# Optimization experiments

Measured on AMD Instinct MI355X. Metric: run time of the kernel, lower is better.

Reference implementation:

```python
import jax, jax.numpy as jnp
import numpy as np

DIM = 768
HEADS = 12
HEAD_DIM = DIM // HEADS
SCALE = HEAD_DIM ** -0.5


def setup_inputs() -> dict:
    key = jax.random.key(0)
    k1, k2, k3, k4, k5 = jax.random.split(key, 5)
    B, N, C = 8, 1024, DIM
    x = jax.random.normal(k1, (B, N, C), dtype=jnp.float32)
    scale_emb = jax.random.normal(k2, (1, 1, C), dtype=jnp.float32)
    # nn.Linear weights stored as (out, in); bias only on proj
    w_qkv = jax.random.normal(k3, (3 * C, C), dtype=jnp.float32) * (C ** -0.5)
    w_proj = jax.random.normal(k4, (C, C), dtype=jnp.float32) * (C ** -0.5)
    b_proj = jax.random.normal(k5, (C,), dtype=jnp.float32) * 0.01
    return {"x": x, "scale_emb": scale_emb, "w_qkv": w_qkv, "w_proj": w_proj, "b_proj": b_proj}


def reference(x, scale_emb, w_qkv, w_proj, b_proj):
    B, N, C = x.shape
    H, D = HEADS, HEAD_DIM
    # qkv: (B, N, 3C) -> (3, B, H, N, D)
    qkv = jnp.einsum('bnc,oc->bno', x, w_qkv)
    qkv = qkv.reshape(B, N, 3, H, D).transpose(2, 0, 3, 1, 4)
    q, k, v = qkv[0], qkv[1], qkv[2]
    # scale_emb broadcast to (B, H, N, D) and added to k
    se = jnp.broadcast_to(scale_emb, (B, N, C)).reshape(B, N, H, D).transpose(0, 2, 1, 3)
    k = k + se
    attn_logits = jnp.einsum('bhnd,bhmd->bhnm', q, k) * SCALE
    attn_probs = jax.nn.softmax(attn_logits, axis=-1)
    out = jnp.einsum('bhnm,bhmd->bhnd', attn_probs, v)
    out = out.transpose(0, 2, 1, 3).reshape(B, N, C)
    out = jnp.einsum('bnc,oc->bno', out, w_proj) + b_proj
    return out, attn_probs
```

## Files before the change

kernel.cpp:

```cpp
#include <hip/hip_runtime.h>
#include <hip/hip_bf16.h>


typedef unsigned short u16;
typedef __attribute__((ext_vector_type(8))) short bf16x8;
typedef __attribute__((ext_vector_type(4))) float f32x4;

#define DEVI static __device__ __forceinline__

DEVI u16 f2bf(float f) {
  union { float f; unsigned int u; } v; v.f = f;
  return (u16)((v.u + 0x7fffu + ((v.u >> 16) & 1u)) >> 16);
}

DEVI void gload16(const void* g, void* l) {
  __builtin_amdgcn_global_load_lds(
      (const __attribute__((address_space(1))) unsigned int*)g,
      (__attribute__((address_space(3))) unsigned int*)l, 16, 0, 0);
}

__global__ void cvt_f32_bf16(const float* __restrict__ src, u16* __restrict__ dst, int n4) {
  int i = blockIdx.x * 256 + threadIdx.x;
  if (i >= n4) return;
  float4 f = ((const float4*)src)[i];
  unsigned int lo = f2bf(f.x) | ((unsigned int)f2bf(f.y) << 16);
  unsigned int hi = f2bf(f.z) | ((unsigned int)f2bf(f.w) << 16);
  ((uint2*)dst)[i] = make_uint2(lo, hi);
}

template<int MODE>
__global__ __launch_bounds__(256)
void gemm128(const u16* __restrict__ A, const u16* __restrict__ Bw, int K,
             const float* __restrict__ se,
             u16* __restrict__ qo, u16* __restrict__ ko, u16* __restrict__ vto,
             const float* __restrict__ bias, float* __restrict__ out)
{
  __shared__ u16 lA[128 * 32];
  __shared__ u16 lB[128 * 32];
  const int mt = blockIdx.x, nt = blockIdx.y;
  const int t = threadIdx.x;
  const int w = t >> 6, l = t & 63, lhi = l >> 4, llo = l & 15;
  const int wr = w >> 1, wc = w & 1;

  f32x4 acc[4][4];
#pragma unroll
  for (int m = 0; m < 4; ++m)
#pragma unroll
    for (int n = 0; n < 4; ++n) acc[m][n] = f32x4{0.f, 0.f, 0.f, 0.f};

  const size_t arow0 = (size_t)mt * 128, brow0 = (size_t)nt * 128;

  for (int k0 = 0; k0 < K; k0 += 32) {
#pragma unroll
    for (int r = 0; r < 2; ++r) {
      int idx = r * 256 + t;
      int row = idx >> 2, col = (idx & 3) * 8;
      gload16(A + (arow0 + row) * K + k0 + col, &lA[idx * 8]);
      gload16(Bw + (brow0 + row) * K + k0 + col, &lB[idx * 8]);
    }
    __syncthreads();
    bf16x8 af[4], bfr[4];
#pragma unroll
    for (int m = 0; m < 4; ++m)
      af[m] = *(const bf16x8*)&lA[(wr * 64 + m * 16 + llo) * 32 + lhi * 8];
#pragma unroll
    for (int n = 0; n < 4; ++n)
      bfr[n] = *(const bf16x8*)&lB[(wc * 64 + n * 16 + llo) * 32 + lhi * 8];
#pragma unroll
    for (int m = 0; m < 4; ++m)
#pragma unroll
      for (int n = 0; n < 4; ++n)
        acc[m][n] = __builtin_amdgcn_mfma_f32_16x16x32_bf16(af[m], bfr[n], acc[m][n], 0, 0, 0);
    __syncthreads();
  }

  if (MODE == 0) {
    const int part = nt / 6;
#pragma unroll
    for (int n = 0; n < 4; ++n) {
      const int gcol = (int)brow0 + wc * 64 + n * 16 + llo;
      const int c = gcol - part * 768;
      const int h = c >> 6, d = c & 63;
      const float sev = (part == 1) ? se[c] : 0.f;
#pragma unroll
      for (int m = 0; m < 4; ++m) {
#pragma unroll
        for (int j = 0; j < 4; ++j) {
          const int tok = (int)arow0 + wr * 64 + m * 16 + lhi * 4 + j;
          const int b = tok >> 10, ntok = tok & 1023;
          const size_t bhh = (size_t)(b * 12 + h);
          const float v = acc[m][n][j];
          if (part == 0)      qo[(bhh * 1024 + ntok) * 64 + d] = f2bf(v * 0.125f);
          else if (part == 1) ko[(bhh * 1024 + ntok) * 64 + d] = f2bf(v + sev);
          else                vto[(bhh * 64 + d) * 1024 + ntok] = f2bf(v);
        }
      }
    }
  } else {
#pragma unroll
    for (int m = 0; m < 4; ++m)
#pragma unroll
      for (int j = 0; j < 4; ++j) {
        const int tok = (int)arow0 + wr * 64 + m * 16 + lhi * 4 + j;
#pragma unroll
        for (int n = 0; n < 4; ++n) {
          const int gcol = (int)brow0 + wc * 64 + n * 16 + llo;
          out[(size_t)tok * 768 + gcol] = acc[m][n][j] + bias[gcol];
        }
      }
  }
}

__global__ __launch_bounds__(256)
void attn_sm(const u16* __restrict__ q, const u16* __restrict__ kin,
             float* __restrict__ probs)
{
  __shared__ u16 lq[32 * 64];
  __shared__ u16 lk[256 * 64];
  __shared__ float red[4][32];
  const int qt = blockIdx.x, bh = blockIdx.y;
  const int t = threadIdx.x;
  const int w = t >> 6, l = t & 63, lhi = l >> 4, llo = l & 15;

  gload16(q + ((size_t)bh * 1024 + qt * 32) * 64 + t * 8, &lq[t * 8]);
  __syncthreads();

  bf16x8 aq[2][2];
#pragma unroll
  for (int m = 0; m < 2; ++m)
#pragma unroll
    for (int kc = 0; kc < 2; ++kc)
      aq[m][kc] = *(const bf16x8*)&lq[(m * 16 + llo) * 64 + kc * 32 + lhi * 8];

  f32x4 acc[4][2][4];
#pragma unroll
  for (int c = 0; c < 4; ++c)
#pragma unroll
    for (int m = 0; m < 2; ++m)
#pragma unroll
      for (int n = 0; n < 4; ++n) acc[c][m][n] = f32x4{0.f, 0.f, 0.f, 0.f};

#pragma unroll
  for (int c = 0; c < 4; ++c) {
    __syncthreads();
#pragma unroll
    for (int r = 0; r < 8; ++r) {
      int idx = r * 256 + t;
      int row = idx >> 3;
      int cb = (idx & 7) * 16;
      bf16x8 val = *(const bf16x8*)(kin + ((size_t)bh * 1024 + c * 256 + row) * 64 + (idx & 7) * 8);
      *(bf16x8*)((char*)lk + row * 128 + (cb ^ ((row & 7) << 4))) = val;
    }
    __syncthreads();
#pragma unroll
    for (int n = 0; n < 4; ++n) {
      const int row = w * 64 + n * 16 + llo;
      const char* rp = (const char*)lk + row * 128;
      const int sw = (row & 7) << 4;
      bf16x8 b0 = *(const bf16x8*)(rp + ((lhi * 16) ^ sw));
      bf16x8 b1 = *(const bf16x8*)(rp + ((64 + lhi * 16) ^ sw));
#pragma unroll
      for (int m = 0; m < 2; ++m) {
        acc[c][m][n] = __builtin_amdgcn_mfma_f32_16x16x32_bf16(aq[m][0], b0, acc[c][m][n], 0, 0, 0);
        acc[c][m][n] = __builtin_amdgcn_mfma_f32_16x16x32_bf16(aq[m][1], b1, acc[c][m][n], 0, 0, 0);
      }
    }
  }

  float rmx[2][4];
#pragma unroll
  for (int m = 0; m < 2; ++m)
#pragma unroll
    for (int j = 0; j < 4; ++j) {
      float v = -1e30f;
#pragma unroll
      for (int c = 0; c < 4; ++c)
#pragma unroll
        for (int n = 0; n < 4; ++n) v = fmaxf(v, acc[c][m][n][j]);
      rmx[m][j] = v;
    }
#pragma unroll
  for (int msk = 1; msk < 16; msk <<= 1)
#pragma unroll
    for (int m = 0; m < 2; ++m)
#pragma unroll
      for (int j = 0; j < 4; ++j)
        rmx[m][j] = fmaxf(rmx[m][j], __shfl_xor(rmx[m][j], msk));
  if (llo == 0) {
#pragma unroll
    for (int m = 0; m < 2; ++m)
#pragma unroll
      for (int j = 0; j < 4; ++j) red[w][m * 16 + lhi * 4 + j] = rmx[m][j];
  }
  __syncthreads();
  float fmx[2][4];
#pragma unroll
  for (int m = 0; m < 2; ++m)
#pragma unroll
    for (int j = 0; j < 4; ++j) {
      int r = m * 16 + lhi * 4 + j;
      fmx[m][j] = fmaxf(fmaxf(red[0][r], red[1][r]), fmaxf(red[2][r], red[3][r]));
    }
  __syncthreads();

  float rsm[2][4];
#pragma unroll
  for (int m = 0; m < 2; ++m)
#pragma unroll
    for (int j = 0; j < 4; ++j) rsm[m][j] = 0.f;
#pragma unroll
  for (int c = 0; c < 4; ++c)
#pragma unroll
    for (int n = 0; n < 4; ++n)
#pragma unroll
      for (int m = 0; m < 2; ++m)
#pragma unroll
        for (int j = 0; j < 4; ++j) {
          float e = __expf(acc[c][m][n][j] - fmx[m][j]);
          acc[c][m][n][j] = e;
          rsm[m][j] += e;
        }
#pragma unroll
  for (int msk = 1; msk < 16; msk <<= 1)
#pragma unroll
    for (int m = 0; m < 2; ++m)
#pragma unroll
      for (int j = 0; j < 4; ++j) rsm[m][j] += __shfl_xor(rsm[m][j], msk);
  if (llo == 0) {
#pragma unroll
    for (int m = 0; m < 2; ++m)
#pragma unroll
      for (int j = 0; j < 4; ++j) red[w][m * 16 + lhi * 4 + j] = rsm[m][j];
  }
  __syncthreads();
  float inv[2][4];
#pragma unroll
  for (int m = 0; m < 2; ++m)
#pragma unroll
    for (int j = 0; j < 4; ++j) {
      int r = m * 16 + lhi * 4 + j;
      inv[m][j] = 1.0f / (red[0][r] + red[1][r] + red[2][r] + red[3][r]);
    }

  float* pb = probs + ((size_t)bh * 1024 + qt * 32) * 1024;
#pragma unroll
  for (int c = 0; c < 4; ++c)
#pragma unroll
    for (int n = 0; n < 4; ++n) {
      const int col = c * 256 + w * 64 + n * 16 + llo;
#pragma unroll
      for (int m = 0; m < 2; ++m)
#pragma unroll
        for (int j = 0; j < 4; ++j) {
          const int r = m * 16 + lhi * 4 + j;
          pb[(size_t)r * 1024 + col] = acc[c][m][n][j] * inv[m][j];
        }
    }
}

__global__ __launch_bounds__(256)
void pv_gemm(const float* __restrict__ probs, const u16* __restrict__ vt,
             u16* __restrict__ ao)
{
  const int mt = blockIdx.x, bh = blockIdx.y;
  const int t = threadIdx.x;
  const int w = t >> 6, l = t & 63, lhi = l >> 4, llo = l & 15;
  const int b = bh / 12, h = bh % 12;

  f32x4 acc[2][4];
#pragma unroll
  for (int m = 0; m < 2; ++m)
#pragma unroll
    for (int n = 0; n < 4; ++n) acc[m][n] = f32x4{0.f, 0.f, 0.f, 0.f};

  const float* pb = probs + ((size_t)bh * 1024 + mt * 128 + w * 32) * 1024;
  const u16* vb = vt + (size_t)bh * 65536;

  for (int k0 = 0; k0 < 1024; k0 += 32) {
    bf16x8 a[2], v[4];
#pragma unroll
    for (int m = 0; m < 2; ++m) {
      const float* p = pb + (size_t)(m * 16 + llo) * 1024 + k0 + lhi * 8;
      float4 f0 = *(const float4*)p;
      float4 f1 = *(const float4*)(p + 4);
      bf16x8 r;
      r[0] = (short)f2bf(f0.x); r[1] = (short)f2bf(f0.y);
      r[2] = (short)f2bf(f0.z); r[3] = (short)f2bf(f0.w);
      r[4] = (short)f2bf(f1.x); r[5] = (short)f2bf(f1.y);
      r[6] = (short)f2bf(f1.z); r[7] = (short)f2bf(f1.w);
      a[m] = r;
    }
#pragma unroll
    for (int n = 0; n < 4; ++n)
      v[n] = *(const bf16x8*)(vb + (size_t)(n * 16 + llo) * 1024 + k0 + lhi * 8);
#pragma unroll
    for (int m = 0; m < 2; ++m)
#pragma unroll
      for (int n = 0; n < 4; ++n)
        acc[m][n] = __builtin_amdgcn_mfma_f32_16x16x32_bf16(a[m], v[n], acc[m][n], 0, 0, 0);
  }
#pragma unroll
  for (int m = 0; m < 2; ++m)
#pragma unroll
    for (int n = 0; n < 4; ++n)
#pragma unroll
      for (int j = 0; j < 4; ++j) {
        const int ntok = mt * 128 + w * 32 + m * 16 + lhi * 4 + j;
        const int d = n * 16 + llo;
        ao[((size_t)(b * 1024 + ntok)) * 768 + h * 64 + d] = f2bf(acc[m][n][j]);
      }
}

extern "C" void kernel_launch(void* const* d_in, const int* in_sizes, int n_in,
                              void* d_out, int out_size, void* d_ws, size_t ws_size,
                              hipStream_t stream) {
  const float* x     = (const float*)d_in[0];
  const float* se    = (const float*)d_in[1];
  const float* wqkv  = (const float*)d_in[2];
  const float* wproj = (const float*)d_in[3];
  const float* bproj = (const float*)d_in[4];
  float* out = (float*)d_out;
  float* probs = out + 6291456;

  if (ws_size < 67633152) return;
  char* ws = (char*)d_ws;
  u16* xb     = (u16*)(ws);
  u16* wqkvb  = (u16*)(ws + 12582912);
  u16* wprojb = (u16*)(ws + 16121856);
  u16* qb     = (u16*)(ws + 17301504);
  u16* kb     = (u16*)(ws + 29884416);
  u16* vtb    = (u16*)(ws + 42467328);
  u16* aob    = (u16*)(ws + 55050240);

  cvt_f32_bf16<<<6144, 256, 0, stream>>>(x, xb, 1572864);
  cvt_f32_bf16<<<1728, 256, 0, stream>>>(wqkv, wqkvb, 442368);
  cvt_f32_bf16<<<576, 256, 0, stream>>>(wprojb == nullptr ? wproj : wproj, wprojb, 147456);
  gemm128<0><<<dim3(64, 18), 256, 0, stream>>>(xb, wqkvb, 768, se, qb, kb, vtb, nullptr, nullptr);
  attn_sm<<<dim3(32, 96), 256, 0, stream>>>(qb, kb, probs);
  pv_gemm<<<dim3(8, 96), 256, 0, stream>>>(probs, vtb, aob);
  gemm128<1><<<dim3(64, 6), 256, 0, stream>>>(aob, wprojb, 768, nullptr, nullptr, nullptr, nullptr, bproj, out);
}
```

Measured before the change: 746.7 us.

## Fuse PV GEMM into softmax kernel using LDS-staged bf16 probabilities

The separate pv_gemm kernel, which re-read the full fp32 probability matrix from global memory, is removed. The softmax kernel now writes each normalized probability both to the output and, as bf16, into a padded LDS tile. It then multiplies that tile by V directly with MFMA, one 256-key chunk at a time, and writes the attention output. This avoids a large global read of probs and one kernel launch, at the cost of extra LDS, extra barriers, and V loads straight from global memory inside the kernel.

```diff
diff --git a/kernel.cpp b/kernel.cpp
--- a/kernel.cpp
+++ b/kernel.cpp
@@ -112,11 +112,13 @@
 }
 
 __global__ __launch_bounds__(256)
-void attn_sm(const u16* __restrict__ q, const u16* __restrict__ kin,
-             float* __restrict__ probs)
+void attn_fused(const u16* __restrict__ q, const u16* __restrict__ kin,
+                const u16* __restrict__ vt, float* __restrict__ probs,
+                u16* __restrict__ ao)
 {
   __shared__ u16 lq[32 * 64];
   __shared__ u16 lk[256 * 64];
+  __shared__ u16 lp[32 * 264];
   __shared__ float red[4][32];
   const int qt = blockIdx.x, bh = blockIdx.y;
   const int t = threadIdx.x;
@@ -242,73 +244,48 @@
       inv[m][j] = 1.0f / (red[0][r] + red[1][r] + red[2][r] + red[3][r]);
     }
 
+  const int b = bh / 12, h = bh % 12;
+  const u16* vb = vt + (size_t)bh * 65536;
   float* pb = probs + ((size_t)bh * 1024 + qt * 32) * 1024;
-#pragma unroll
-  for (int c = 0; c < 4; ++c)
+  f32x4 acco[2];
+  acco[0] = f32x4{0.f, 0.f, 0.f, 0.f};
+  acco[1] = f32x4{0.f, 0.f, 0.f, 0.f};
+
+#pragma unroll
+  for (int c = 0; c < 4; ++c) {
+    __syncthreads();
 #pragma unroll
     for (int n = 0; n < 4; ++n) {
-      const int col = c * 256 + w * 64 + n * 16 + llo;
+      const int kloc = w * 64 + n * 16 + llo;
 #pragma unroll
       for (int m = 0; m < 2; ++m)
 #pragma unroll
         for (int j = 0; j < 4; ++j) {
           const int r = m * 16 + lhi * 4 + j;
-          pb[(size_t)r * 1024 + col] = acc[c][m][n][j] * inv[m][j];
+          const float p = acc[c][m][n][j] * inv[m][j];
+          pb[(size_t)r * 1024 + c * 256 + kloc] = p;
+          lp[r * 264 + kloc] = f2bf(p);
         }
     }
-}
-
-__global__ __launch_bounds__(256)
-void pv_gemm(const float* __restrict__ probs, const u16* __restrict__ vt,
-             u16* __restrict__ ao)
-{
-  const int mt = blockIdx.x, bh = blockIdx.y;
-  const int t = threadIdx.x;
-  const int w = t >> 6, l = t & 63, lhi = l >> 4, llo = l & 15;
-  const int b = bh / 12, h = bh % 12;
-
-  f32x4 acc[2][4];
-#pragma unroll
-  for (int m = 0; m < 2; ++m)
-#pragma unroll
-    for (int n = 0; n < 4; ++n) acc[m][n] = f32x4{0.f, 0.f, 0.f, 0.f};
-
-  const float* pb = probs + ((size_t)bh * 1024 + mt * 128 + w * 32) * 1024;
-  const u16* vb = vt + (size_t)bh * 65536;
-
-  for (int k0 = 0; k0 < 1024; k0 += 32) {
-    bf16x8 a[2], v[4];
-#pragma unroll
-    for (int m = 0; m < 2; ++m) {
-      const float* p = pb + (size_t)(m * 16 + llo) * 1024 + k0 + lhi * 8;
-      float4 f0 = *(const float4*)p;
-      float4 f1 = *(const float4*)(p + 4);
-      bf16x8 r;
-      r[0] = (short)f2bf(f0.x); r[1] = (short)f2bf(f0.y);
-      r[2] = (short)f2bf(f0.z); r[3] = (short)f2bf(f0.w);
-      r[4] = (short)f2bf(f1.x); r[5] = (short)f2bf(f1.y);
-      r[6] = (short)f2bf(f1.z); r[7] = (short)f2bf(f1.w);
-      a[m] = r;
-    }
-#pragma unroll
-    for (int n = 0; n < 4; ++n)
-      v[n] = *(const bf16x8*)(vb + (size_t)(n * 16 + llo) * 1024 + k0 + lhi * 8);
-#pragma unroll
-    for (int m = 0; m < 2; ++m)
-#pragma unroll
-      for (int n = 0; n < 4; ++n)
-        acc[m][n] = __builtin_amdgcn_mfma_f32_16x16x32_bf16(a[m], v[n], acc[m][n], 0, 0, 0);
-  }
-#pragma unroll
-  for (int m = 0; m < 2; ++m)
-#pragma unroll
-    for (int n = 0; n < 4; ++n)
-#pragma unroll
-      for (int j = 0; j < 4; ++j) {
-        const int ntok = mt * 128 + w * 32 + m * 16 + lhi * 4 + j;
-        const int d = n * 16 + llo;
-        ao[((size_t)(b * 1024 + ntok)) * 768 + h * 64 + d] = f2bf(acc[m][n][j]);
-      }
+    __syncthreads();
+#pragma unroll
+    for (int ks = 0; ks < 8; ++ks) {
+      bf16x8 a0 = *(const bf16x8*)&lp[llo * 264 + ks * 32 + lhi * 8];
+      bf16x8 a1 = *(const bf16x8*)&lp[(16 + llo) * 264 + ks * 32 + lhi * 8];
+      bf16x8 v = *(const bf16x8*)(vb + (size_t)(w * 16 + llo) * 1024 + c * 256 + ks * 32 + lhi * 8);
+      acco[0] = __builtin_amdgcn_mfma_f32_16x16x32_bf16(a0, v, acco[0], 0, 0, 0);
+      acco[1] = __builtin_amdgcn_mfma_f32_16x16x32_bf16(a1, v, acco[1], 0, 0, 0);
+    }
+  }
+
+#pragma unroll
+  for (int m = 0; m < 2; ++m)
+#pragma unroll
+    for (int j = 0; j < 4; ++j) {
+      const int ntok = qt * 32 + m * 16 + lhi * 4 + j;
+      const int d = w * 16 + llo;
+      ao[((size_t)(b * 1024 + ntok)) * 768 + h * 64 + d] = f2bf(acco[m][j]);
+    }
 }
 
 extern "C" void kernel_launch(void* const* d_in, const int* in_sizes, int n_in,
@@ -334,9 +311,8 @@
 
   cvt_f32_bf16<<<6144, 256, 0, stream>>>(x, xb, 1572864);
   cvt_f32_bf16<<<1728, 256, 0, stream>>>(wqkv, wqkvb, 442368);
-  cvt_f32_bf16<<<576, 256, 0, stream>>>(wprojb == nullptr ? wproj : wproj, wprojb, 147456);
+  cvt_f32_bf16<<<576, 256, 0, stream>>>(wproj, wprojb, 147456);
   gemm128<0><<<dim3(64, 18), 256, 0, stream>>>(xb, wqkvb, 768, se, qb, kb, vtb, nullptr, nullptr);
-  attn_sm<<<dim3(32, 96), 256, 0, stream>>>(qb, kb, probs);
-  pv_gemm<<<dim3(8, 96), 256, 0, stream>>>(probs, vtb, aob);
+  attn_fused<<<dim3(32, 96), 256, 0, stream>>>(qb, kb, vtb, probs, aob);
   gemm128<1><<<dim3(64, 6), 256, 0, stream>>>(aob, wprojb, 768, nullptr, nullptr, nullptr, nullptr, bproj, out);
 }
```

Result: faster. 724.5 us (-3.0%).
